# Performance work log

Measured on AMD Instinct MI355X. Metric: run time of the kernel, lower is better.

The kernel has to match this reference:

```python
import jax, jax.numpy as jnp
import numpy as np

N_NODES = 100000
N_FEAT = 256
N_HIDDEN = 64
N_EDGES = 3200000
LEAKY_SLOPE = 0.05


def setup_inputs() -> dict:
    key = jax.random.key(0)
    k1, k2, k3, k4, k5 = jax.random.split(key, 5)
    x = jax.random.normal(k1, (N_NODES, N_FEAT), dtype=jnp.float32)
    edge_index = jax.random.randint(k2, (2, N_EDGES), 0, N_NODES, dtype=jnp.int64)
    # params (torch Linear default-like scale)
    W_fc = jax.random.normal(k3, (N_FEAT, N_HIDDEN), dtype=jnp.float32) / np.sqrt(N_FEAT)
    a_w = jax.random.normal(k4, (2 * N_HIDDEN, 1), dtype=jnp.float32) / np.sqrt(2 * N_HIDDEN)
    a_b = jax.random.normal(k5, (1,), dtype=jnp.float32) * 0.01
    return {"x": x, "edge_index": edge_index, "W_fc": W_fc, "a_w": a_w, "a_b": a_b}


def reference(x, edge_index, W_fc, a_w, a_b):
    n = x.shape[0]
    h = x @ W_fc                                  # [N, H]
    src = edge_index[0]
    dst = edge_index[1]
    # a([h_src, h_dst]) == h_src @ a_w[:H] + h_dst @ a_w[H:] + a_b (same math, avoids concat)
    s = h @ a_w[:N_HIDDEN, 0]                     # [N]
    t = h @ a_w[N_HIDDEN:, 0]                     # [N]
    e = s[src] + t[dst] + a_b[0]                  # [E]
    e = jnp.where(e >= 0, e, LEAKY_SLOPE * e)     # LeakyReLU(0.05)
    attention = jnp.exp(e)                        # [E]
    row_sum = jax.ops.segment_sum(attention, src, num_segments=n)  # [N]
    alpha = attention / row_sum[src]              # [E]
    # sparse mm: out[i] = sum_{e: src_e=i} alpha_e * h[dst_e]
    out = jax.ops.segment_sum(alpha[:, None] * h[dst], src, num_segments=n)  # [N, H]
    return out, alpha
```

## Files before the change

### kernel.cpp

```cpp
#include <hip/hip_runtime.h>
#include <hip/hip_fp16.h>
#include <cstdint>
#include <cstddef>

#define NFEAT 256
#define NHID 64
#define SLOPE 0.05f
#define NBKT_MAX 392
#define P1 256
#define DSTBITS 17
#define WTPAD 264

typedef _Float16 half8 __attribute__((ext_vector_type(8)));
typedef float f32x4 __attribute__((ext_vector_type(4)));

__global__ __launch_bounds__(256) void fc_kernel(
    const float* __restrict__ x, const float* __restrict__ W,
    const float* __restrict__ aw,
    __half* __restrict__ h, float* __restrict__ srinv, float* __restrict__ t,
    int nNodes)
{
    __shared__ _Float16 Wt[NHID][WTPAD];

    const int tid = threadIdx.x;

    #pragma unroll 4
    for (int it = 0; it < 16; ++it) {
        const int idx = it * 256 + tid;
        const int n  = idx & 63;
        const int k0 = (idx >> 6) << 2;
        union { _Float16 v[4]; uint2 u; } pk;
        pk.v[0] = (_Float16)W[(k0 + 0) * NHID + n];
        pk.v[1] = (_Float16)W[(k0 + 1) * NHID + n];
        pk.v[2] = (_Float16)W[(k0 + 2) * NHID + n];
        pk.v[3] = (_Float16)W[(k0 + 3) * NHID + n];
        *(uint2*)&Wt[n][k0] = pk.u;
    }
    __syncthreads();

    const int l   = tid & 63;
    const int wv  = tid >> 6;
    const int l16 = l & 15;
    const int q   = l >> 4;
    const int kb8 = q * 8;

    const int blockRow = blockIdx.x * 128;
    const int nClamp = nNodes - 1;
    const int r0c = min(blockRow + wv * 32 + l16,      nClamp);
    const int r1c = min(blockRow + wv * 32 + l16 + 16, nClamp);
    const float* xr0 = x + (size_t)r0c * NFEAT;
    const float* xr1 = x + (size_t)r1c * NFEAT;

    f32x4 acc[2][4];
    #pragma unroll
    for (int m = 0; m < 2; ++m)
        #pragma unroll
        for (int nb = 0; nb < 4; ++nb)
            acc[m][nb] = (f32x4){0.f, 0.f, 0.f, 0.f};

    #pragma unroll
    for (int ks = 0; ks < 8; ++ks) {
        const int k0 = ks * 32 + kb8;
        const float4 fa0 = *(const float4*)(xr0 + k0);
        const float4 fa1 = *(const float4*)(xr0 + k0 + 4);
        const float4 fb0 = *(const float4*)(xr1 + k0);
        const float4 fb1 = *(const float4*)(xr1 + k0 + 4);
        half8 a0, a1;
        a0[0] = (_Float16)fa0.x; a0[1] = (_Float16)fa0.y;
        a0[2] = (_Float16)fa0.z; a0[3] = (_Float16)fa0.w;
        a0[4] = (_Float16)fa1.x; a0[5] = (_Float16)fa1.y;
        a0[6] = (_Float16)fa1.z; a0[7] = (_Float16)fa1.w;
        a1[0] = (_Float16)fb0.x; a1[1] = (_Float16)fb0.y;
        a1[2] = (_Float16)fb0.z; a1[3] = (_Float16)fb0.w;
        a1[4] = (_Float16)fb1.x; a1[5] = (_Float16)fb1.y;
        a1[6] = (_Float16)fb1.z; a1[7] = (_Float16)fb1.w;
        const half8 b0 = *(const half8*)&Wt[ 0 + l16][k0];
        const half8 b1 = *(const half8*)&Wt[16 + l16][k0];
        const half8 b2 = *(const half8*)&Wt[32 + l16][k0];
        const half8 b3 = *(const half8*)&Wt[48 + l16][k0];
        acc[0][0] = __builtin_amdgcn_mfma_f32_16x16x32_f16(a0, b0, acc[0][0], 0, 0, 0);
        acc[0][1] = __builtin_amdgcn_mfma_f32_16x16x32_f16(a0, b1, acc[0][1], 0, 0, 0);
        acc[0][2] = __builtin_amdgcn_mfma_f32_16x16x32_f16(a0, b2, acc[0][2], 0, 0, 0);
        acc[0][3] = __builtin_amdgcn_mfma_f32_16x16x32_f16(a0, b3, acc[0][3], 0, 0, 0);
        acc[1][0] = __builtin_amdgcn_mfma_f32_16x16x32_f16(a1, b0, acc[1][0], 0, 0, 0);
        acc[1][1] = __builtin_amdgcn_mfma_f32_16x16x32_f16(a1, b1, acc[1][1], 0, 0, 0);
        acc[1][2] = __builtin_amdgcn_mfma_f32_16x16x32_f16(a1, b2, acc[1][2], 0, 0, 0);
        acc[1][3] = __builtin_amdgcn_mfma_f32_16x16x32_f16(a1, b3, acc[1][3], 0, 0, 0);
    }

    const float aws0 = aw[l16],      aws1 = aw[16 + l16];
    const float aws2 = aw[32 + l16], aws3 = aw[48 + l16];
    const float awt0 = aw[64 + l16], awt1 = aw[80 + l16];
    const float awt2 = aw[96 + l16], awt3 = aw[112 + l16];

    #pragma unroll
    for (int m = 0; m < 2; ++m) {
        const int rb = blockRow + wv * 32 + m * 16 + q * 4;
        #pragma unroll
        for (int r = 0; r < 4; ++r) {
            const int row = rb + r;
            const bool ok = row < nNodes;
            const float c0 = acc[m][0][r];
            const float c1 = acc[m][1][r];
            const float c2 = acc[m][2][r];
            const float c3 = acc[m][3][r];
            if (ok) {
                __half* hp = &h[(size_t)row * NHID + l16];
                hp[0]  = __float2half(c0);
                hp[16] = __float2half(c1);
                hp[32] = __float2half(c2);
                hp[48] = __float2half(c3);
            }
            float ps = c0 * aws0 + c1 * aws1 + c2 * aws2 + c3 * aws3;
            float pt = c0 * awt0 + c1 * awt1 + c2 * awt2 + c3 * awt3;
            ps += __shfl_xor(ps, 1, 16); pt += __shfl_xor(pt, 1, 16);
            ps += __shfl_xor(ps, 2, 16); pt += __shfl_xor(pt, 2, 16);
            ps += __shfl_xor(ps, 4, 16); pt += __shfl_xor(pt, 4, 16);
            ps += __shfl_xor(ps, 8, 16); pt += __shfl_xor(pt, 8, 16);
            if (ok && l16 == 0) { srinv[2 * row] = ps; t[row] = pt; }
        }
    }
}

__global__ __launch_bounds__(256) void cnt_kernel(
    const int* __restrict__ ei, int E, int CPB, int nbkt, int* __restrict__ cntT)
{
    __shared__ int hist[NBKT_MAX];
    const int g = blockIdx.x;
    const int tid = threadIdx.x;
    for (int i = tid; i < nbkt; i += 256) hist[i] = 0;
    __syncthreads();
    const int beg = g * CPB;
    const int end = min(E, beg + CPB);
    const int c4 = (end - beg) >> 2;
    for (int i = tid; i < c4; i += 256) {
        const int4 v = *(const int4*)&ei[beg + i * 4];
        atomicAdd(&hist[v.x >> 8], 1);
        atomicAdd(&hist[v.y >> 8], 1);
        atomicAdd(&hist[v.z >> 8], 1);
        atomicAdd(&hist[v.w >> 8], 1);
    }
    for (int e = beg + c4 * 4 + tid; e < end; e += 256)
        atomicAdd(&hist[ei[e] >> 8], 1);
    __syncthreads();
    for (int b = tid; b < nbkt; b += 256)
        cntT[b * P1 + g] = hist[b];
}

__global__ __launch_bounds__(256) void scanA_kernel(
    const int* __restrict__ v, int* __restrict__ bsum, int n)
{
    __shared__ int sh[256];
    const int i = blockIdx.x * 256 + threadIdx.x;
    sh[threadIdx.x] = (i < n) ? v[i] : 0;
    __syncthreads();
    #pragma unroll
    for (int off = 128; off > 0; off >>= 1) {
        if (threadIdx.x < off) sh[threadIdx.x] += sh[threadIdx.x + off];
        __syncthreads();
    }
    if (threadIdx.x == 0) bsum[blockIdx.x] = sh[0];
}

__global__ __launch_bounds__(256) void scanB_kernel(
    const int* __restrict__ bsum, int* __restrict__ bscan, int NB)
{
    __shared__ int sh[512];
    const int tid = threadIdx.x;
    sh[tid] = (tid < NB) ? bsum[tid] : 0;
    sh[256 + tid] = (256 + tid < NB) ? bsum[256 + tid] : 0;
    __syncthreads();
    if (tid == 0) {
        int run = 0;
        for (int i = 0; i < NB; ++i) { int v = sh[i]; sh[i] = run; run += v; }
    }
    __syncthreads();
    if (tid < NB) bscan[tid] = sh[tid];
    if (256 + tid < NB) bscan[256 + tid] = sh[256 + tid];
}

__global__ __launch_bounds__(256) void scanC_kernel(
    const int* __restrict__ v, const int* __restrict__ bscan,
    int* __restrict__ outp, int n)
{
    __shared__ int sh[256];
    const int tid = threadIdx.x;
    const int i = blockIdx.x * 256 + tid;
    const int val = (i < n) ? v[i] : 0;
    sh[tid] = val;
    __syncthreads();
    #pragma unroll
    for (int off = 1; off < 256; off <<= 1) {
        int add = (tid >= off) ? sh[tid - off] : 0;
        __syncthreads();
        sh[tid] += add;
        __syncthreads();
    }
    const int incl = sh[tid];
    const int base = bscan[blockIdx.x];
    if (i < n) outp[i] = base + incl - val;
    if (i == n - 1) outp[n] = base + incl;
}

__global__ __launch_bounds__(256) void place_kernel(
    const int* __restrict__ ei, int E, int CPB, int nbkt,
    const int* __restrict__ base, int* __restrict__ pairs)
{
    __shared__ int cur[NBKT_MAX];
    const int g = blockIdx.x;
    const int tid = threadIdx.x;
    for (int b = tid; b < nbkt; b += 256) cur[b] = base[b * P1 + g];
    __syncthreads();
    const int beg = g * CPB;
    const int end = min(E, beg + CPB);
    const int c4 = (end - beg) >> 2;
    for (int i = tid; i < c4; i += 256) {
        const int e = beg + i * 4;
        const int4 s4 = *(const int4*)&ei[e];
        const int4 d4 = *(const int4*)&ei[E + e];
        int p;
        p = atomicAdd(&cur[s4.x >> 8], 1); pairs[p] = ((s4.x & 255) << DSTBITS) | d4.x;
        p = atomicAdd(&cur[s4.y >> 8], 1); pairs[p] = ((s4.y & 255) << DSTBITS) | d4.y;
        p = atomicAdd(&cur[s4.z >> 8], 1); pairs[p] = ((s4.z & 255) << DSTBITS) | d4.z;
        p = atomicAdd(&cur[s4.w >> 8], 1); pairs[p] = ((s4.w & 255) << DSTBITS) | d4.w;
    }
    for (int e = beg + c4 * 4 + tid; e < end; e += 256) {
        const int sn = ei[e];
        const int d  = ei[E + e];
        const int pos = atomicAdd(&cur[sn >> 8], 1);
        pairs[pos] = ((sn & 255) << DSTBITS) | d;
    }
}

__global__ __launch_bounds__(512) void bsort_kernel(
    const int* __restrict__ pairs, const int* __restrict__ base,
    int* __restrict__ offsets, int* __restrict__ sdst,
    int nNodes, int nbkt, int E)
{
    __shared__ int cnt[256];
    __shared__ int off[256];
    __shared__ int cur[256];

    const int bkt = blockIdx.x;
    const int tid = threadIdx.x;
    const int beg = base[bkt * P1];
    const int end = (bkt + 1 < nbkt) ? base[(bkt + 1) * P1] : E;

    if (tid < 256) cnt[tid] = 0;
    __syncthreads();

    for (int e = beg + tid; e < end; e += 512)
        atomicAdd(&cnt[pairs[e] >> DSTBITS], 1);
    __syncthreads();

    if (tid < 256) off[tid] = cnt[tid];
    __syncthreads();
    #pragma unroll
    for (int o = 1; o < 256; o <<= 1) {
        int v = 0;
        if (tid < 256 && tid >= o) v = off[tid - o];
        __syncthreads();
        if (tid < 256) off[tid] += v;
        __syncthreads();
    }
    if (tid < 256) {
        const int ex = off[tid] - cnt[tid];
        cur[tid] = ex;
        const int n = (bkt << 8) + tid;
        if (n < nNodes) offsets[n] = beg + ex;
    }
    if (tid == 0 && bkt == nbkt - 1) offsets[nNodes] = E;
    __syncthreads();

    for (int e = beg + tid; e < end; e += 512) {
        const int p = pairs[e];
        const int pos = beg + atomicAdd(&cur[p >> DSTBITS], 1);
        sdst[pos] = p & ((1 << DSTBITS) - 1);
    }
}

__global__ __launch_bounds__(256) void agg_kernel(
    const int* __restrict__ offsets, const int* __restrict__ sdst,
    float* __restrict__ srinv, const float* __restrict__ t,
    const __half* __restrict__ h, const float* __restrict__ ab_p,
    float* __restrict__ out, int nNodes)
{
    const int lane = threadIdx.x & 63;
    const int wv = threadIdx.x >> 6;
    const int quarter = lane >> 4;
    const int col = lane & 15;
    const float ab = ab_p[0];
    const int stride = gridDim.x * 4;
    const uint2* hh4 = (const uint2*)h;

    for (int n = blockIdx.x * 4 + wv; n < nNodes; n += stride) {
        const int beg = offsets[n];
        const int end = offsets[n + 1];
        const float sn = srinv[2 * n];
        float part = 0.f;
        float4 acc = {0.f, 0.f, 0.f, 0.f};
        for (int i0 = beg; i0 < end; i0 += 64) {
            const int my = min(end - i0, 64);
            int dl = 0; float el = 0.f;
            if (lane < my) {
                dl = sdst[i0 + lane];
                float ev = sn + t[dl] + ab;
                ev = (ev >= 0.f) ? ev : SLOPE * ev;
                el = __expf(ev);
            }
            part += el;
            const int my4 = (my + 3) & ~3;
            int j = 0;
            for (; j + 8 <= my4; j += 8) {
                const int   d0 = __shfl(dl, j + quarter);
                const float e0 = __shfl(el, j + quarter);
                const int   d1 = __shfl(dl, j + 4 + quarter);
                const float e1 = __shfl(el, j + 4 + quarter);
                const uint2 r0 = hh4[(size_t)d0 * 16 + col];
                const uint2 r1 = hh4[(size_t)d1 * 16 + col];
                const float2 lo0 = __half22float2(*(const __half2*)&r0.x);
                const float2 hi0 = __half22float2(*(const __half2*)&r0.y);
                const float2 lo1 = __half22float2(*(const __half2*)&r1.x);
                const float2 hi1 = __half22float2(*(const __half2*)&r1.y);
                acc.x += e0 * lo0.x; acc.y += e0 * lo0.y;
                acc.z += e0 * hi0.x; acc.w += e0 * hi0.y;
                acc.x += e1 * lo1.x; acc.y += e1 * lo1.y;
                acc.z += e1 * hi1.x; acc.w += e1 * hi1.y;
            }
            for (; j < my4; j += 4) {
                const int   d0 = __shfl(dl, j + quarter);
                const float e0 = __shfl(el, j + quarter);
                const uint2 r0 = hh4[(size_t)d0 * 16 + col];
                const float2 lo0 = __half22float2(*(const __half2*)&r0.x);
                const float2 hi0 = __half22float2(*(const __half2*)&r0.y);
                acc.x += e0 * lo0.x; acc.y += e0 * lo0.y;
                acc.z += e0 * hi0.x; acc.w += e0 * hi0.y;
            }
        }
        #pragma unroll
        for (int off = 32; off > 0; off >>= 1) part += __shfl_xor(part, off, 64);
        const float inv = (end > beg) ? 1.0f / part : 0.f;
        if (lane == 0) srinv[2 * n + 1] = inv;
        acc.x += __shfl_xor(acc.x, 16, 64); acc.x += __shfl_xor(acc.x, 32, 64);
        acc.y += __shfl_xor(acc.y, 16, 64); acc.y += __shfl_xor(acc.y, 32, 64);
        acc.z += __shfl_xor(acc.z, 16, 64); acc.z += __shfl_xor(acc.z, 32, 64);
        acc.w += __shfl_xor(acc.w, 16, 64); acc.w += __shfl_xor(acc.w, 32, 64);
        if (quarter == 0) {
            float4 o;
            o.x = acc.x * inv; o.y = acc.y * inv;
            o.z = acc.z * inv; o.w = acc.w * inv;
            *(float4*)&out[(size_t)n * NHID + col * 4] = o;
        }
    }
}

__global__ __launch_bounds__(256) void alpha_kernel(
    const int* __restrict__ ei, const float* __restrict__ srinv,
    const float* __restrict__ t,
    const float* __restrict__ ab_p, float* __restrict__ alpha, int E)
{
    const float ab = ab_p[0];
    const int gid = blockIdx.x * blockDim.x + threadIdx.x;
    const int step = gridDim.x * blockDim.x;
    const int E4 = E >> 2;

    #define AEDGE(sn, d) ({                                                 \
        const float2 sr = *(const float2*)&srinv[2 * (sn)];                 \
        float ev = sr.x + t[d] + ab;                                        \
        ev = (ev >= 0.f) ? ev : SLOPE * ev;                                 \
        __expf(ev) * sr.y; })

    for (int i = gid; i < E4; i += step) {
        const int e = i * 4;
        const int4 s4 = *(const int4*)&ei[e];
        const int4 d4 = *(const int4*)&ei[E + e];
        float4 a;
        a.x = AEDGE(s4.x, d4.x);
        a.y = AEDGE(s4.y, d4.y);
        a.z = AEDGE(s4.z, d4.z);
        a.w = AEDGE(s4.w, d4.w);
        *(float4*)&alpha[e] = a;
    }
    for (int e = E4 * 4 + gid; e < E; e += step) {
        const int sn = ei[e];
        const int d = ei[E + e];
        alpha[e] = AEDGE(sn, d);
    }
}

extern "C" void kernel_launch(void* const* d_in, const int* in_sizes, int n_in,
                              void* d_out, int out_size, void* d_ws, size_t ws_size,
                              hipStream_t stream)
{
    const float* x  = (const float*)d_in[0];
    const int*   ei = (const int*)d_in[1];
    const float* W  = (const float*)d_in[2];
    const float* aw = (const float*)d_in[3];
    const float* ab = (const float*)d_in[4];

    const int nNodes = in_sizes[0] / NFEAT;
    const int E      = in_sizes[1] / 2;
    const int NBfc   = (nNodes + 127) / 128;
    const int nbkt   = (nNodes + 255) >> 8;
    const int CPB    = ((E + P1 - 1) / P1 + 3) & ~3;
    const int nScan  = nbkt * P1;
    const int NBs    = (nScan + 255) / 256;

    float* out   = (float*)d_out;
    float* alpha = out + (size_t)nNodes * NHID;

    __half* h      = (__half*)d_ws;
    float* srinv   = (float*)(h + (size_t)nNodes * NHID);
    float* t       = srinv + 2 * nNodes;
    int*   cntT    = (int*)(t + nNodes);
    int*   base    = cntT + nScan;
    int*   bsum    = base + nScan + 4;
    int*   bscan   = bsum + NBs;
    int*   offsets = bscan + NBs;
    int*   sdst    = offsets + nNodes + 4;
    int*   pairs   = sdst + E;

    fc_kernel<<<NBfc, 256, 0, stream>>>(x, W, aw, h, srinv, t, nNodes);
    cnt_kernel<<<P1, 256, 0, stream>>>(ei, E, CPB, nbkt, cntT);
    scanA_kernel<<<NBs, 256, 0, stream>>>(cntT, bsum, nScan);
    scanB_kernel<<<1, 256, 0, stream>>>(bsum, bscan, NBs);
    scanC_kernel<<<NBs, 256, 0, stream>>>(cntT, bscan, base, nScan);
    place_kernel<<<P1, 256, 0, stream>>>(ei, E, CPB, nbkt, base, pairs);
    bsort_kernel<<<nbkt, 512, 0, stream>>>(pairs, base, offsets, sdst,
                                           nNodes, nbkt, E);
    agg_kernel<<<2048, 256, 0, stream>>>(offsets, sdst, srinv, t, h, ab,
                                         out, nNodes);
    alpha_kernel<<<2048, 256, 0, stream>>>(ei, srinv, t, ab, alpha, E);
}
```

Measured before the change: 179.2 us.

## Stage bucket scatter in LDS and fold scan-of-block-sums into scanC

Doubles the number of partition chunks so each place block handles fewer edges, then has place_kernel sort its chunk into shared memory by bucket before writing contiguous runs to the global pairs array, making global stores coalesced instead of scattered. The single-block scanB kernel is removed; each scanC block instead sums the preceding block sums itself. This cuts one launch and the random global writes, at the cost of a 25KB shared buffer per block (lower occupancy), a serial per-block prefix loop, a binary search per element, and redundant bsum reads that grow with the number of blocks.

New measurement: 175.3 us. 2.2% less time.

```diff
diff --git a/kernel.cpp b/kernel.cpp
--- a/kernel.cpp
+++ b/kernel.cpp
@@ -7,9 +7,10 @@
 #define NHID 64
 #define SLOPE 0.05f
 #define NBKT_MAX 392
-#define P1 256
+#define P1 512
 #define DSTBITS 17
 #define WTPAD 264
+#define SORTBUF 6272
 
 typedef _Float16 half8 __attribute__((ext_vector_type(8)));
 typedef float f32x4 __attribute__((ext_vector_type(4)));
@@ -162,29 +163,28 @@
     if (threadIdx.x == 0) bsum[blockIdx.x] = sh[0];
 }
 
-__global__ __launch_bounds__(256) void scanB_kernel(
-    const int* __restrict__ bsum, int* __restrict__ bscan, int NB)
-{
-    __shared__ int sh[512];
+__global__ __launch_bounds__(256) void scanC_kernel(
+    const int* __restrict__ v, const int* __restrict__ bsum,
+    int* __restrict__ outp, int n, int NB)
+{
+    __shared__ int red[256];
+    __shared__ int sh[256];
+    __shared__ int base0s;
     const int tid = threadIdx.x;
-    sh[tid] = (tid < NB) ? bsum[tid] : 0;
-    sh[256 + tid] = (256 + tid < NB) ? bsum[256 + tid] : 0;
-    __syncthreads();
-    if (tid == 0) {
-        int run = 0;
-        for (int i = 0; i < NB; ++i) { int v = sh[i]; sh[i] = run; run += v; }
-    }
-    __syncthreads();
-    if (tid < NB) bscan[tid] = sh[tid];
-    if (256 + tid < NB) bscan[256 + tid] = sh[256 + tid];
-}
-
-__global__ __launch_bounds__(256) void scanC_kernel(
-    const int* __restrict__ v, const int* __restrict__ bscan,
-    int* __restrict__ outp, int n)
-{
-    __shared__ int sh[256];
-    const int tid = threadIdx.x;
+
+    int partial = 0;
+    for (int j = tid; j < (int)blockIdx.x; j += 256) partial += bsum[j];
+    red[tid] = partial;
+    __syncthreads();
+    #pragma unroll
+    for (int off = 128; off > 0; off >>= 1) {
+        if (tid < off) red[tid] += red[tid + off];
+        __syncthreads();
+    }
+    if (tid == 0) base0s = red[0];
+    __syncthreads();
+    const int base0 = base0s;
+
     const int i = blockIdx.x * 256 + tid;
     const int val = (i < n) ? v[i] : 0;
     sh[tid] = val;
@@ -197,38 +197,67 @@
         __syncthreads();
     }
     const int incl = sh[tid];
-    const int base = bscan[blockIdx.x];
-    if (i < n) outp[i] = base + incl - val;
-    if (i == n - 1) outp[n] = base + incl;
+    if (i < n) outp[i] = base0 + incl - val;
+    if (i == n - 1) outp[n] = base0 + incl;
 }
 
 __global__ __launch_bounds__(256) void place_kernel(
     const int* __restrict__ ei, int E, int CPB, int nbkt,
-    const int* __restrict__ base, int* __restrict__ pairs)
-{
+    const int* __restrict__ cntT, const int* __restrict__ base,
+    int* __restrict__ pairs)
+{
+    __shared__ int loff[NBKT_MAX + 1];
     __shared__ int cur[NBKT_MAX];
+    __shared__ int gb[NBKT_MAX];
+    __shared__ int sorted[SORTBUF];
+
     const int g = blockIdx.x;
     const int tid = threadIdx.x;
-    for (int b = tid; b < nbkt; b += 256) cur[b] = base[b * P1 + g];
-    __syncthreads();
     const int beg = g * CPB;
     const int end = min(E, beg + CPB);
-    const int c4 = (end - beg) >> 2;
+    const int total = end - beg;
+
+    for (int b = tid; b < nbkt; b += 256) {
+        loff[b] = cntT[b * P1 + g];
+        gb[b]   = base[b * P1 + g];
+    }
+    __syncthreads();
+    if (tid == 0) {
+        int run = 0;
+        for (int b = 0; b < nbkt; ++b) { const int c = loff[b]; loff[b] = run; run += c; }
+        loff[nbkt] = run;
+    }
+    __syncthreads();
+    for (int b = tid; b < nbkt; b += 256) cur[b] = loff[b];
+    __syncthreads();
+
+    const int c4 = total >> 2;
     for (int i = tid; i < c4; i += 256) {
         const int e = beg + i * 4;
         const int4 s4 = *(const int4*)&ei[e];
         const int4 d4 = *(const int4*)&ei[E + e];
         int p;
-        p = atomicAdd(&cur[s4.x >> 8], 1); pairs[p] = ((s4.x & 255) << DSTBITS) | d4.x;
-        p = atomicAdd(&cur[s4.y >> 8], 1); pairs[p] = ((s4.y & 255) << DSTBITS) | d4.y;
-        p = atomicAdd(&cur[s4.z >> 8], 1); pairs[p] = ((s4.z & 255) << DSTBITS) | d4.z;
-        p = atomicAdd(&cur[s4.w >> 8], 1); pairs[p] = ((s4.w & 255) << DSTBITS) | d4.w;
+        p = atomicAdd(&cur[s4.x >> 8], 1); sorted[p] = ((s4.x & 255) << DSTBITS) | d4.x;
+        p = atomicAdd(&cur[s4.y >> 8], 1); sorted[p] = ((s4.y & 255) << DSTBITS) | d4.y;
+        p = atomicAdd(&cur[s4.z >> 8], 1); sorted[p] = ((s4.z & 255) << DSTBITS) | d4.z;
+        p = atomicAdd(&cur[s4.w >> 8], 1); sorted[p] = ((s4.w & 255) << DSTBITS) | d4.w;
     }
     for (int e = beg + c4 * 4 + tid; e < end; e += 256) {
         const int sn = ei[e];
         const int d  = ei[E + e];
-        const int pos = atomicAdd(&cur[sn >> 8], 1);
-        pairs[pos] = ((sn & 255) << DSTBITS) | d;
+        const int p  = atomicAdd(&cur[sn >> 8], 1);
+        sorted[p] = ((sn & 255) << DSTBITS) | d;
+    }
+    __syncthreads();
+
+    for (int i = tid; i < total; i += 256) {
+        int lo = 0, hi = nbkt;
+        #pragma unroll
+        for (int it = 0; it < 9; ++it) {
+            const int mid = (lo + hi) >> 1;
+            if (loff[mid] <= i) lo = mid; else hi = mid;
+        }
+        pairs[gb[lo] + (i - loff[lo])] = sorted[i];
     }
 }
 
@@ -415,17 +444,15 @@
     int*   cntT    = (int*)(t + nNodes);
     int*   base    = cntT + nScan;
     int*   bsum    = base + nScan + 4;
-    int*   bscan   = bsum + NBs;
-    int*   offsets = bscan + NBs;
+    int*   offsets = bsum + NBs;
     int*   sdst    = offsets + nNodes + 4;
     int*   pairs   = sdst + E;
 
     fc_kernel<<<NBfc, 256, 0, stream>>>(x, W, aw, h, srinv, t, nNodes);
     cnt_kernel<<<P1, 256, 0, stream>>>(ei, E, CPB, nbkt, cntT);
     scanA_kernel<<<NBs, 256, 0, stream>>>(cntT, bsum, nScan);
-    scanB_kernel<<<1, 256, 0, stream>>>(bsum, bscan, NBs);
-    scanC_kernel<<<NBs, 256, 0, stream>>>(cntT, bscan, base, nScan);
-    place_kernel<<<P1, 256, 0, stream>>>(ei, E, CPB, nbkt, base, pairs);
+    scanC_kernel<<<NBs, 256, 0, stream>>>(cntT, bsum, base, nScan, NBs);
+    place_kernel<<<P1, 256, 0, stream>>>(ei, E, CPB, nbkt, cntT, base, pairs);
     bsort_kernel<<<nbkt, 512, 0, stream>>>(pairs, base, offsets, sdst,
                                            nNodes, nbkt, E);
     agg_kernel<<<2048, 256, 0, stream>>>(offsets, sdst, srinv, t, h, ab,
```
